# Optimization experiments

Hardware: AMD Instinct MI355X
Metric: run time of the kernel (lower is better)

## Reference

```python
import jax, jax.numpy as jnp
import numpy as np

K = 3            # kernel_size
S = 4            # up_factor
VMAX = 1.0
TAU = 0.5
CENTER_BIAS = 2.5
SMOOTH_RES = 0.15
C_IN = 21
HIDDEN = 48
B_, H0, W0 = 4, 81, 81
CTR = K // 2      # = 1, also GL recursion depth M


def _dir_step_diff(k):
    """Precompute (base_pos - base_neg) per direction/step: [8, M+1, k, k]."""
    c = k // 2
    dirs = np.array([[1, 0], [1, 1], [0, 1], [-1, 1], [-1, 0], [-1, -1], [0, -1], [1, -1]], np.float32)
    dirs = dirs / (np.linalg.norm(dirs, axis=1, keepdims=True) + 1e-8)
    yy, xx = np.meshgrid(np.arange(k), np.arange(k), indexing='ij')
    rel = np.stack([yy - c, xx - c], -1).astype(np.float32)
    diff = np.zeros((8, c + 1, k, k), np.float32)
    for d in range(8):
        v = dirs[d]
        proj = rel[..., 0] * v[1] + rel[..., 1] * v[0]
        step = np.clip(np.round(proj), -c, c).astype(np.int64)
        for m in range(c + 1):
            diff[d, m] = (step == m).astype(np.float32) - (step == -m).astype(np.float32)
    return diff

DIFF = jnp.asarray(_dir_step_diff(K))  # [8, M+1, K, K]


def conv3x3(x, w, b):
    y = jax.lax.conv_general_dilated(x, w, (1, 1), 'SAME',
                                     dimension_numbers=('NCHW', 'OIHW', 'NCHW'))
    return y + b[None, :, None, None]


def bilinear_up(x, s):
    """F.interpolate(scale_factor=s, mode='bilinear', align_corners=True)."""
    B, C, h, w = x.shape
    H, W = h * s, w * s
    ys = jnp.linspace(0.0, h - 1.0, H)
    xs = jnp.linspace(0.0, w - 1.0, W)
    y0 = jnp.clip(jnp.floor(ys).astype(jnp.int32), 0, h - 2)
    x0 = jnp.clip(jnp.floor(xs).astype(jnp.int32), 0, w - 2)
    wy = (ys - y0)[:, None]
    wx = (xs - x0)[None, :]
    x00 = x[:, :, y0][:, :, :, x0]
    x01 = x[:, :, y0][:, :, :, x0 + 1]
    x10 = x[:, :, y0 + 1][:, :, :, x0]
    x11 = x[:, :, y0 + 1][:, :, :, x0 + 1]
    return (x00 * (1 - wy) * (1 - wx) + x01 * (1 - wy) * wx
            + x10 * wy * (1 - wx) + x11 * wy * wx)


def setup_inputs() -> dict:
    key = jax.random.key(0)
    ks = jax.random.split(key, 6)
    wn = lambda k, shape: jax.random.normal(k, shape, jnp.float32) * 0.05
    return {
        'x': jax.random.normal(ks[0], (B_, C_IN, H0, W0), jnp.float32),
        'w1o': wn(ks[1], (HIDDEN, C_IN, 3, 3)), 'b1o': jnp.zeros((HIDDEN,), jnp.float32),
        'w2o': wn(ks[2], (8, HIDDEN, 3, 3)), 'b2o': jnp.zeros((8,), jnp.float32),
        'w1g': wn(ks[3], (HIDDEN, C_IN, 3, 3)), 'b1g': jnp.zeros((HIDDEN,), jnp.float32),
        'w2g': wn(ks[4], (1, HIDDEN, 3, 3)), 'b2g': jnp.zeros((1,), jnp.float32),
        'beta': jnp.asarray(1.6, jnp.float32),
    }


def reference(x, w1o, b1o, w2o, b2o, w1g, b1g, w2g, b2g, beta):
    B, C, h, w = x.shape
    c = CTR
    # heads
    raw_v = conv3x3(jax.nn.relu(conv3x3(x, w1o, b1o)), w2o, b2o)          # [B,8,h,w]
    g = jax.nn.sigmoid(conv3x3(jax.nn.relu(conv3x3(x, w1g, b1g)), w2g, b2g))  # [B,1,h,w]
    v = VMAX * jnp.tanh(raw_v)
    # Gruenwald-Letnikov coefficients, M = center (=1 for k=3)
    coeffs = [jnp.ones_like(v)]
    wm = coeffs[0]
    for m in range(1, c + 1):
        wm = wm * (v - m + 1.0) / m * -1.0
        coeffs.append(wm)
    coeff = jnp.stack(coeffs, axis=2)                                      # [B,8,M+1,h,w]
    # direction kernels, averaged over the 8 directions
    ker = jnp.einsum('bdmhw,dmkl->bklhw', coeff, DIFF) / 8.0               # [B,K,K,h,w]
    mask_pre = ker.reshape(B, K * K, h, w)
    ci = c * K + c
    # NOTE: torch adds center_bias in-place on a view of ker -> ker itself is biased too
    mask_pre = mask_pre.at[:, ci].add(CENTER_BIAS)
    ker_b = mask_pre.reshape(B, K, K, h, w)
    mask_lp = jax.nn.softmax(mask_pre / TAU, axis=1)                       # [B,9,h,w]
    # unfold 3x3 window with reflect padding
    xp = jnp.pad(x, ((0, 0), (0, 0), (c, c), (c, c)), mode='reflect')
    patches = jnp.stack([xp[:, :, i:i + h, j:j + w]
                         for i in range(K) for j in range(K)], axis=2)     # [B,C,9,h,w]
    rep2 = lambda a, ax: jnp.repeat(jnp.repeat(a, S, axis=ax), S, axis=ax + 1)
    neigh = rep2(patches, 3)                                               # [B,C,9,H,W]
    mask_lp_u = rep2(mask_lp, 2)                                           # [B,9,H,W]
    g_up = rep2(g, 2)                                                      # [B,1,H,W]
    x_up = bilinear_up(x, S)                                               # [B,C,H,W]
    y_lp_out = jnp.einsum('bcnHW,bnHW->bcHW', neigh, mask_lp_u)
    lam = SMOOTH_RES * (1.0 - g_up)
    y_lp = x_up + lam * (y_lp_out - x_up)
    # highpass branch (mode='both')
    ker_hp = ker_b - ker_b.mean(axis=(1, 2), keepdims=True)
    ker_hp = ker_hp / (jnp.abs(ker_hp).sum(axis=(1, 2), keepdims=True) + 1e-8)
    mask_hp = rep2(ker_hp.reshape(B, K * K, h, w), 2)
    y_hp = jnp.einsum('bcnHW,bnHW->bcHW', neigh, mask_hp)
    y = y_lp + jnp.tanh(beta) * g_up * y_hp
    return (y, v, g_up)
```

## Files before the change

### kernel.cpp

```cpp
#include <hip/hip_runtime.h>
#include <math.h>

#define B_N   4
#define CIN   21
#define HIDC  48
#define H0    81
#define NP    6561
#define HH    324
#define NPH   104976

__device__ __forceinline__ float tanh_fast(float x) {
    float e = __expf(2.f * x);
    return 1.f - 2.f / (e + 1.f);
}

__global__ __launch_bounds__(256) void k1_conv1(
    const float* __restrict__ x,
    const float* __restrict__ w1o, const float* __restrict__ b1o,
    const float* __restrict__ w1g, const float* __restrict__ b1g,
    float* __restrict__ hid_o, float* __restrict__ hid_g)
{
    __shared__ __align__(16) float wt[189 * 12];
    __shared__ float bs[12];
    const int tid = threadIdx.x;
    const int grp = blockIdx.y;
    const int b   = blockIdx.z;
    const bool head_o = (grp < 4);
    const int ocb = (grp & 3) * 12;
    const float* wsrc = head_o ? w1o : w1g;
    for (int i = tid; i < 189 * 12; i += 256) {
        const int ict = i / 12, oc = i - ict * 12;
        wt[i] = wsrc[(ocb + oc) * 189 + ict];
    }
    if (tid < 12) bs[tid] = (head_o ? b1o : b1g)[ocb + tid];
    __syncthreads();

    const int px = blockIdx.x * 256 + tid;
    const bool valid = (px < NP);
    const int oy = px / H0, ox = px - oy * H0;
    const float* xb = x + (size_t)b * CIN * NP;

    float acc[12];
    #pragma unroll
    for (int j = 0; j < 12; j++) acc[j] = bs[j];

    for (int ic = 0; ic < CIN; ic++) {
        const float* xc = xb + ic * NP;
        float xv[9];
        #pragma unroll
        for (int ky = 0; ky < 3; ky++) {
            const int iy = oy + ky - 1;
            const bool rok = valid && ((unsigned)iy < (unsigned)H0);
            #pragma unroll
            for (int kx = 0; kx < 3; kx++) {
                const int ix = ox + kx - 1;
                const bool ok = rok && ((unsigned)ix < (unsigned)H0);
                xv[ky * 3 + kx] = ok ? xc[iy * H0 + ix] : 0.f;
            }
        }
        #pragma unroll
        for (int tap = 0; tap < 9; tap++) {
            const float4 w0 = *(const float4*)&wt[(ic * 9 + tap) * 12];
            const float4 w1 = *(const float4*)&wt[(ic * 9 + tap) * 12 + 4];
            const float4 w2 = *(const float4*)&wt[(ic * 9 + tap) * 12 + 8];
            const float wj[12] = {w0.x, w0.y, w0.z, w0.w, w1.x, w1.y, w1.z, w1.w,
                                  w2.x, w2.y, w2.z, w2.w};
            const float xvt = xv[tap];
            #pragma unroll
            for (int j = 0; j < 12; j++) acc[j] = fmaf(xvt, wj[j], acc[j]);
        }
    }

    if (valid) {
        float* outp = (head_o ? hid_o : hid_g) + ((size_t)b * HIDC + ocb) * NP + px;
        #pragma unroll
        for (int j = 0; j < 12; j++) outp[j * NP] = fmaxf(acc[j], 0.f);
    }
}

__global__ __launch_bounds__(256) void k2_conv2_masks(
    const float* __restrict__ hid_o, const float* __restrict__ hid_g,
    const float* __restrict__ w2o, const float* __restrict__ b2o,
    const float* __restrict__ w2g, const float* __restrict__ b2g,
    float* __restrict__ v_out,
    float* __restrict__ g_buf, float* __restrict__ m_lp, float* __restrict__ m_hp)
{
    __shared__ __align__(16) float wo_s[HIDC * 9 * 8];
    __shared__ float wg_s[HIDC * 9];
    __shared__ float red[4][32][12];
    __shared__ float res_s[32][28];
    const int tid = threadIdx.x;
    const int b = blockIdx.y;

    for (int i = tid; i < HIDC * 9 * 8; i += 256) {
        const int d = i / (HIDC * 9), r = i - d * (HIDC * 9);
        wo_s[r * 8 + d] = w2o[i];
    }
    for (int i = tid; i < HIDC * 9; i += 256) wg_s[i] = w2g[i];
    __syncthreads();

    const int pxl = tid & 31;
    const int s   = tid >> 5;
    const int w   = tid >> 6;
    const int px  = blockIdx.x * 32 + pxl;
    const bool valid = (px < NP);
    const int oy = px / H0, ox = px - oy * H0;
    const int ic0 = s * 6;
    const float* po = hid_o + ((size_t)b * HIDC + ic0) * NP;
    const float* pg = hid_g + ((size_t)b * HIDC + ic0) * NP;

    float a[8] = {0.f, 0.f, 0.f, 0.f, 0.f, 0.f, 0.f, 0.f};
    float ag = 0.f;

    #pragma unroll 1
    for (int ky = 0; ky < 3; ky++) {
        const int iy = oy + ky - 1;
        const bool rok = valid && ((unsigned)iy < (unsigned)H0);
        #pragma unroll
        for (int kx = 0; kx < 3; kx++) {
            const int ix = ox + kx - 1;
            const bool ok = rok && ((unsigned)ix < (unsigned)H0);
            const int off = iy * H0 + ix;
            const int tap = ky * 3 + kx;
            #pragma unroll
            for (int j = 0; j < 6; j++) {
                const float vo = ok ? po[j * NP + off] : 0.f;
                const float vg = ok ? pg[j * NP + off] : 0.f;
                const int wb = ((ic0 + j) * 9 + tap) * 8;
                const float4 wA = *(const float4*)&wo_s[wb];
                const float4 wB = *(const float4*)&wo_s[wb + 4];
                a[0] = fmaf(vo, wA.x, a[0]); a[1] = fmaf(vo, wA.y, a[1]);
                a[2] = fmaf(vo, wA.z, a[2]); a[3] = fmaf(vo, wA.w, a[3]);
                a[4] = fmaf(vo, wB.x, a[4]); a[5] = fmaf(vo, wB.y, a[5]);
                a[6] = fmaf(vo, wB.z, a[6]); a[7] = fmaf(vo, wB.w, a[7]);
                ag = fmaf(vg, wg_s[(ic0 + j) * 9 + tap], ag);
            }
        }
    }

    #pragma unroll
    for (int n = 0; n < 8; n++) a[n] += __shfl_xor(a[n], 32);
    ag += __shfl_xor(ag, 32);
    if ((tid & 32) == 0) {
        #pragma unroll
        for (int n = 0; n < 8; n++) red[w][pxl][n] = a[n];
        red[w][pxl][8] = ag;
    }
    __syncthreads();

    if (tid < 32 && valid) {
        float v[8];
        #pragma unroll
        for (int n = 0; n < 8; n++)
            v[n] = tanh_fast(red[0][tid][n] + red[1][tid][n] + red[2][tid][n]
                             + red[3][tid][n] + b2o[n]);
        const float agf = red[0][tid][8] + red[1][tid][8] + red[2][tid][8]
                        + red[3][tid][8] + b2g[0];
        const float g = 1.f / (1.f + __expf(-agf));

        constexpr float DT[8][9] = {
            {-1, 0, 1, -1, 0, 1, -1, 0, 1},
            {-1,-1, 0, -1, 0, 1,  0, 1, 1},
            {-1,-1,-1,  0, 0, 0,  1, 1, 1},
            { 0,-1,-1,  1, 0,-1,  1, 1, 0},
            { 1, 0,-1,  1, 0,-1,  1, 0,-1},
            { 1, 1, 0,  1, 0,-1,  0,-1,-1},
            { 1, 1, 1,  0, 0, 0, -1,-1,-1},
            { 0, 1, 1, -1, 0, 1, -1,-1, 0}};
        float ker[9];
        #pragma unroll
        for (int n = 0; n < 9; n++) {
            float t = 0.f;
            #pragma unroll
            for (int d = 0; d < 8; d++) t += v[d] * DT[d][n];
            ker[n] = -0.125f * t;
        }
        ker[4] += 2.5f;
        float mx = ker[0];
        #pragma unroll
        for (int n = 1; n < 9; n++) mx = fmaxf(mx, ker[n]);
        float exn[9], sum = 0.f;
        #pragma unroll
        for (int n = 0; n < 9; n++) { exn[n] = __expf((ker[n] - mx) * 2.0f); sum += exn[n]; }
        const float rs = 1.f / sum;
        float mean = 0.f;
        #pragma unroll
        for (int n = 0; n < 9; n++) mean += ker[n];
        mean *= (1.f / 9.f);
        float den = 1e-8f;
        #pragma unroll
        for (int n = 0; n < 9; n++) den += fabsf(ker[n] - mean);
        const float rd = 1.f / den;

        #pragma unroll
        for (int n = 0; n < 8; n++) res_s[tid][n] = v[n];
        res_s[tid][8] = g;
        #pragma unroll
        for (int n = 0; n < 9; n++) {
            res_s[tid][9 + n]  = exn[n] * rs;
            res_s[tid][18 + n] = (ker[n] - mean) * rd;
        }
    }
    __syncthreads();

    const int px0 = blockIdx.x * 32;
    for (int j = tid; j < 27 * 32; j += 256) {
        const int plane = j >> 5, pl = j & 31;
        const int p = px0 + pl;
        if (p >= NP) continue;
        const float val = res_s[pl][plane];
        float* dst;
        if (plane < 8)        dst = v_out + ((size_t)b * 8 + plane) * NP;
        else if (plane == 8)  dst = g_buf + (size_t)b * NP;
        else if (plane < 18)  dst = m_lp + ((size_t)b * 9 + (plane - 9)) * NP;
        else                  dst = m_hp + ((size_t)b * 9 + (plane - 18)) * NP;
        dst[p] = val;
    }
}

__global__ __launch_bounds__(256) void k4_up(
    const float* __restrict__ x, const float* __restrict__ g_buf,
    const float* __restrict__ m_lp, const float* __restrict__ m_hp,
    const float* __restrict__ beta,
    float* __restrict__ y_out, float* __restrict__ gup_out)
{
    __shared__ float ml_s[9][81];
    __shared__ float mh_s[9][81];
    __shared__ float g_s[81];
    __shared__ float xrow[3][11][84];
    __shared__ float alp_s[11][84];
    __shared__ float ahp_s[11][84];
    const int tid  = threadIdx.x;
    const int h0r  = blockIdx.x;
    const int ygrp = blockIdx.y;
    const int b    = blockIdx.z;
    const int c0   = ygrp * 11;
    const int nc   = (ygrp == 0) ? 11 : 10;

    const int rb = h0r * H0;
    for (int i = tid; i < 19 * 81; i += 256) {
        const int pl = i / 81, wq = i - pl * 81;
        if (pl < 9)       ml_s[pl][wq] = m_lp[((size_t)b * 9 + pl) * NP + rb + wq];
        else if (pl < 18) mh_s[pl - 9][wq] = m_hp[((size_t)b * 9 + (pl - 9)) * NP + rb + wq];
        else              g_s[wq] = g_buf[(size_t)b * NP + rb + wq];
    }
    const int r0 = (h0r == 0) ? 1 : h0r - 1;
    const int r2 = (h0r == H0 - 1) ? H0 - 2 : h0r + 1;
    const int rr[3] = {r0, h0r, r2};
    for (int i = tid; i < 3 * nc * 81; i += 256) {
        const int t = i / (nc * 81), rem = i - t * nc * 81;
        const int cc = rem / 81, wq = rem - cc * 81;
        xrow[t][cc][wq] = x[((size_t)b * CIN + c0 + cc) * NP + rr[t] * H0 + wq];
    }
    __syncthreads();

    for (int i = tid; i < nc * 81; i += 256) {
        const int cc = i / 81, wq = i - cc * 81;
        const int xm = (wq == 0) ? 1 : wq - 1;
        const int xp = (wq == H0 - 1) ? H0 - 2 : wq + 1;
        float alp = 0.f, ahp = 0.f;
        #pragma unroll
        for (int t = 0; t < 3; t++) {
            const float p0 = xrow[t][cc][xm];
            const float p1 = xrow[t][cc][wq];
            const float p2 = xrow[t][cc][xp];
            alp += p0 * ml_s[t * 3 + 0][wq] + p1 * ml_s[t * 3 + 1][wq] + p2 * ml_s[t * 3 + 2][wq];
            ahp += p0 * mh_s[t * 3 + 0][wq] + p1 * mh_s[t * 3 + 1][wq] + p2 * mh_s[t * 3 + 2][wq];
        }
        alp_s[cc][wq] = alp;
        ahp_s[cc][wq] = ahp;
    }
    __syncthreads();

    const float tb = tanh_fast(beta[0]);
    for (int i = tid; i < 11 * 4 * 81; i += 256) {
        const int pl = i / 324, rem = i - pl * 324;
        const int dh = rem / 81, wq = rem - dh * 81;
        const int H = h0r * 4 + dh;
        if (ygrp == 1 && pl == 10) {
            const float g = g_s[wq];
            *reinterpret_cast<float4*>(gup_out + (size_t)b * NPH + H * HH + wq * 4) =
                make_float4(g, g, g, g);
            continue;
        }
        const int cc = pl;
        const int c = c0 + pl;
        const float g = g_s[wq];
        const float lam = 0.15f * (1.f - g);
        const float gh = tb * g;
        const float alp = alp_s[cc][wq];
        const float ahp = ahp_s[cc][wq];
        const float ysf = (float)H * (80.f / 323.f);
        int y0 = (int)ysf;
        if (y0 > H0 - 2) y0 = H0 - 2;
        const float wy = ysf - (float)y0;
        const int sy = y0 - h0r + 1;
        const int xm = (wq == 0) ? 1 : wq - 1;
        const int xp = (wq == H0 - 1) ? H0 - 2 : wq + 1;
        const float a0 = xrow[sy][cc][(wq == 0) ? 0 : xm];
        const float a1 = xrow[sy][cc][wq];
        const float a2 = xrow[sy][cc][(wq == H0 - 1) ? H0 - 1 : xp];
        const float b0 = xrow[sy + 1][cc][(wq == 0) ? 0 : xm];
        const float b1 = xrow[sy + 1][cc][wq];
        const float b2 = xrow[sy + 1][cc][(wq == H0 - 1) ? H0 - 1 : xp];
        float res[4];
        #pragma unroll
        for (int k = 0; k < 4; k++) {
            const int W = wq * 4 + k;
            const float xsf = (float)W * (80.f / 323.f);
            int x0 = (int)xsf;
            if (x0 > H0 - 2) x0 = H0 - 2;
            const float wx = xsf - (float)x0;
            const int sx = x0 - wq + 1;
            const float top = (sx == 0) ? a0 + (a1 - a0) * wx : a1 + (a2 - a1) * wx;
            const float bot = (sx == 0) ? b0 + (b1 - b0) * wx : b1 + (b2 - b1) * wx;
            const float xup = top + (bot - top) * wy;
            res[k] = xup + lam * (alp - xup) + gh * ahp;
        }
        *reinterpret_cast<float4*>(y_out + ((size_t)b * CIN + c) * NPH + H * HH + wq * 4) =
            make_float4(res[0], res[1], res[2], res[3]);
    }
}

extern "C" void kernel_launch(void* const* d_in, const int* in_sizes, int n_in,
                              void* d_out, int out_size, void* d_ws, size_t ws_size,
                              hipStream_t stream)
{
    const float* x    = (const float*)d_in[0];
    const float* w1o  = (const float*)d_in[1];
    const float* b1o  = (const float*)d_in[2];
    const float* w2o  = (const float*)d_in[3];
    const float* b2o  = (const float*)d_in[4];
    const float* w1g  = (const float*)d_in[5];
    const float* b1g  = (const float*)d_in[6];
    const float* w2g  = (const float*)d_in[7];
    const float* b2g  = (const float*)d_in[8];
    const float* beta = (const float*)d_in[9];
    float* out = (float*)d_out;
    float* wsf = (float*)d_ws;

    float* hid_o = wsf;
    float* hid_g = hid_o + (size_t)B_N * HIDC * NP;
    float* m_lp  = hid_g + (size_t)B_N * HIDC * NP;
    float* m_hp  = m_lp + (size_t)B_N * 9 * NP;
    float* g_buf = m_hp + (size_t)B_N * 9 * NP;

    float* y_out = out;
    float* v_out = out + (size_t)B_N * CIN * NPH;
    float* gup   = v_out + (size_t)B_N * 8 * NP;

    k1_conv1<<<dim3((NP + 255) / 256, 8, B_N), 256, 0, stream>>>(
        x, w1o, b1o, w1g, b1g, hid_o, hid_g);
    k2_conv2_masks<<<dim3((NP + 31) / 32, B_N), 256, 0, stream>>>(
        hid_o, hid_g, w2o, b2o, w2g, b2g, v_out, g_buf, m_lp, m_hp);
    k4_up<<<dim3(H0, 2, B_N), 256, 0, stream>>>(x, g_buf, m_lp, m_hp, beta, y_out, gup);
}
```

Measured before the change: 152.8 us.

## Fuse conv2/mask kernel with upsampling kernel per low-res row half

Merges the second conv plus mask computation into the upsampling kernel. Each block now covers one low-res row half (41 pixels) for all 21 channels, so the lp/hp masks and gate stay in shared memory and never go through global workspace. This removes one launch and the global round trip for the masks. In exchange only 246 of 256 threads do conv2 work, and the grid of 648 blocks each reload the conv2 weights and all channel rows, so parallelism and occupancy shift.

```diff
diff --git a/kernel.cpp b/kernel.cpp
--- a/kernel.cpp
+++ b/kernel.cpp
@@ -78,85 +78,103 @@
     }
 }
 
-__global__ __launch_bounds__(256) void k2_conv2_masks(
+__global__ __launch_bounds__(256) void k24_conv2_up(
+    const float* __restrict__ x,
     const float* __restrict__ hid_o, const float* __restrict__ hid_g,
     const float* __restrict__ w2o, const float* __restrict__ b2o,
     const float* __restrict__ w2g, const float* __restrict__ b2g,
-    float* __restrict__ v_out,
-    float* __restrict__ g_buf, float* __restrict__ m_lp, float* __restrict__ m_hp)
+    const float* __restrict__ beta,
+    float* __restrict__ v_out, float* __restrict__ y_out,
+    float* __restrict__ gup_out)
 {
     __shared__ __align__(16) float wo_s[HIDC * 9 * 8];
     __shared__ float wg_s[HIDC * 9];
-    __shared__ float red[4][32][12];
-    __shared__ float res_s[32][28];
-    const int tid = threadIdx.x;
-    const int b = blockIdx.y;
+    __shared__ float xrow[3][CIN][84];
+    __shared__ float red_u[6 * 41 * 9];
+    __shared__ float ml_s[9][41];
+    __shared__ float mh_s[9][41];
+    __shared__ float g_s[41];
+
+    const int tid  = threadIdx.x;
+    const int h0r  = blockIdx.x;
+    const int half = blockIdx.y;
+    const int b    = blockIdx.z;
+    const int wq0  = half * 41;
 
     for (int i = tid; i < HIDC * 9 * 8; i += 256) {
         const int d = i / (HIDC * 9), r = i - d * (HIDC * 9);
         wo_s[r * 8 + d] = w2o[i];
     }
     for (int i = tid; i < HIDC * 9; i += 256) wg_s[i] = w2g[i];
-    __syncthreads();
-
-    const int pxl = tid & 31;
-    const int s   = tid >> 5;
-    const int w   = tid >> 6;
-    const int px  = blockIdx.x * 32 + pxl;
-    const bool valid = (px < NP);
-    const int oy = px / H0, ox = px - oy * H0;
-    const int ic0 = s * 6;
-    const float* po = hid_o + ((size_t)b * HIDC + ic0) * NP;
-    const float* pg = hid_g + ((size_t)b * HIDC + ic0) * NP;
-
-    float a[8] = {0.f, 0.f, 0.f, 0.f, 0.f, 0.f, 0.f, 0.f};
-    float ag = 0.f;
-
-    #pragma unroll 1
-    for (int ky = 0; ky < 3; ky++) {
-        const int iy = oy + ky - 1;
-        const bool rok = valid && ((unsigned)iy < (unsigned)H0);
-        #pragma unroll
-        for (int kx = 0; kx < 3; kx++) {
-            const int ix = ox + kx - 1;
-            const bool ok = rok && ((unsigned)ix < (unsigned)H0);
-            const int off = iy * H0 + ix;
-            const int tap = ky * 3 + kx;
-            #pragma unroll
-            for (int j = 0; j < 6; j++) {
-                const float vo = ok ? po[j * NP + off] : 0.f;
-                const float vg = ok ? pg[j * NP + off] : 0.f;
-                const int wb = ((ic0 + j) * 9 + tap) * 8;
-                const float4 wA = *(const float4*)&wo_s[wb];
-                const float4 wB = *(const float4*)&wo_s[wb + 4];
-                a[0] = fmaf(vo, wA.x, a[0]); a[1] = fmaf(vo, wA.y, a[1]);
-                a[2] = fmaf(vo, wA.z, a[2]); a[3] = fmaf(vo, wA.w, a[3]);
-                a[4] = fmaf(vo, wB.x, a[4]); a[5] = fmaf(vo, wB.y, a[5]);
-                a[6] = fmaf(vo, wB.z, a[6]); a[7] = fmaf(vo, wB.w, a[7]);
-                ag = fmaf(vg, wg_s[(ic0 + j) * 9 + tap], ag);
+
+    const int r0 = (h0r == 0) ? 1 : h0r - 1;
+    const int r2 = (h0r == H0 - 1) ? H0 - 2 : h0r + 1;
+    const int rr[3] = {r0, h0r, r2};
+    for (int i = tid; i < 3 * CIN * H0; i += 256) {
+        const int t3 = i / (CIN * H0), rem = i - t3 * CIN * H0;
+        const int cc = rem / H0, wq = rem - cc * H0;
+        xrow[t3][cc][wq] = x[((size_t)b * CIN + cc) * NP + rr[t3] * H0 + wq];
+    }
+    __syncthreads();
+
+    {
+        const int grp = tid / 41;
+        const int pxl = tid - grp * 41;
+        const int wq  = wq0 + pxl;
+        const bool cactive = (grp < 6) && (wq < H0);
+        if (cactive) {
+            const int ic0 = grp * 8;
+            const float* po = hid_o + ((size_t)b * HIDC + ic0) * NP;
+            const float* pg = hid_g + ((size_t)b * HIDC + ic0) * NP;
+            float a[8] = {0.f, 0.f, 0.f, 0.f, 0.f, 0.f, 0.f, 0.f};
+            float ag = 0.f;
+            #pragma unroll
+            for (int ky = 0; ky < 3; ky++) {
+                const int iy = h0r + ky - 1;
+                const bool rok = ((unsigned)iy < (unsigned)H0);
+                #pragma unroll
+                for (int kx = 0; kx < 3; kx++) {
+                    const int ix = wq + kx - 1;
+                    const bool ok = rok && ((unsigned)ix < (unsigned)H0);
+                    const int off = iy * H0 + ix;
+                    const int tap = ky * 3 + kx;
+                    #pragma unroll
+                    for (int j = 0; j < 8; j++) {
+                        const float vo = ok ? po[j * NP + off] : 0.f;
+                        const float vg = ok ? pg[j * NP + off] : 0.f;
+                        const int wb = ((ic0 + j) * 9 + tap) * 8;
+                        const float4 wA = *(const float4*)&wo_s[wb];
+                        const float4 wB = *(const float4*)&wo_s[wb + 4];
+                        a[0] = fmaf(vo, wA.x, a[0]); a[1] = fmaf(vo, wA.y, a[1]);
+                        a[2] = fmaf(vo, wA.z, a[2]); a[3] = fmaf(vo, wA.w, a[3]);
+                        a[4] = fmaf(vo, wB.x, a[4]); a[5] = fmaf(vo, wB.y, a[5]);
+                        a[6] = fmaf(vo, wB.z, a[6]); a[7] = fmaf(vo, wB.w, a[7]);
+                        ag = fmaf(vg, wg_s[(ic0 + j) * 9 + tap], ag);
+                    }
+                }
             }
-        }
-    }
-
-    #pragma unroll
-    for (int n = 0; n < 8; n++) a[n] += __shfl_xor(a[n], 32);
-    ag += __shfl_xor(ag, 32);
-    if ((tid & 32) == 0) {
-        #pragma unroll
-        for (int n = 0; n < 8; n++) red[w][pxl][n] = a[n];
-        red[w][pxl][8] = ag;
-    }
-    __syncthreads();
-
-    if (tid < 32 && valid) {
+            float* rp = &red_u[(grp * 41 + pxl) * 9];
+            #pragma unroll
+            for (int n = 0; n < 8; n++) rp[n] = a[n];
+            rp[8] = ag;
+        }
+    }
+    __syncthreads();
+
+    if (tid < 41 && (wq0 + tid) < H0) {
+        const int wq = wq0 + tid;
+        float s[9];
+        #pragma unroll
+        for (int n = 0; n < 9; n++) {
+            float t = 0.f;
+            #pragma unroll
+            for (int g = 0; g < 6; g++) t += red_u[(g * 41 + tid) * 9 + n];
+            s[n] = t;
+        }
         float v[8];
         #pragma unroll
-        for (int n = 0; n < 8; n++)
-            v[n] = tanh_fast(red[0][tid][n] + red[1][tid][n] + red[2][tid][n]
-                             + red[3][tid][n] + b2o[n]);
-        const float agf = red[0][tid][8] + red[1][tid][8] + red[2][tid][8]
-                        + red[3][tid][8] + b2g[0];
-        const float g = 1.f / (1.f + __expf(-agf));
+        for (int n = 0; n < 8; n++) v[n] = tanh_fast(s[n] + b2o[n]);
+        const float g = 1.f / (1.f + __expf(-(s[8] + b2g[0])));
 
         constexpr float DT[8][9] = {
             {-1, 0, 1, -1, 0, 1, -1, 0, 1},
@@ -193,103 +211,58 @@
         const float rd = 1.f / den;
 
         #pragma unroll
-        for (int n = 0; n < 8; n++) res_s[tid][n] = v[n];
-        res_s[tid][8] = g;
-        #pragma unroll
         for (int n = 0; n < 9; n++) {
-            res_s[tid][9 + n]  = exn[n] * rs;
-            res_s[tid][18 + n] = (ker[n] - mean) * rd;
-        }
-    }
-    __syncthreads();
-
-    const int px0 = blockIdx.x * 32;
-    for (int j = tid; j < 27 * 32; j += 256) {
-        const int plane = j >> 5, pl = j & 31;
-        const int p = px0 + pl;
-        if (p >= NP) continue;
-        const float val = res_s[pl][plane];
-        float* dst;
-        if (plane < 8)        dst = v_out + ((size_t)b * 8 + plane) * NP;
-        else if (plane == 8)  dst = g_buf + (size_t)b * NP;
-        else if (plane < 18)  dst = m_lp + ((size_t)b * 9 + (plane - 9)) * NP;
-        else                  dst = m_hp + ((size_t)b * 9 + (plane - 18)) * NP;
-        dst[p] = val;
-    }
-}
-
-__global__ __launch_bounds__(256) void k4_up(
-    const float* __restrict__ x, const float* __restrict__ g_buf,
-    const float* __restrict__ m_lp, const float* __restrict__ m_hp,
-    const float* __restrict__ beta,
-    float* __restrict__ y_out, float* __restrict__ gup_out)
-{
-    __shared__ float ml_s[9][81];
-    __shared__ float mh_s[9][81];
-    __shared__ float g_s[81];
-    __shared__ float xrow[3][11][84];
-    __shared__ float alp_s[11][84];
-    __shared__ float ahp_s[11][84];
-    const int tid  = threadIdx.x;
-    const int h0r  = blockIdx.x;
-    const int ygrp = blockIdx.y;
-    const int b    = blockIdx.z;
-    const int c0   = ygrp * 11;
-    const int nc   = (ygrp == 0) ? 11 : 10;
-
-    const int rb = h0r * H0;
-    for (int i = tid; i < 19 * 81; i += 256) {
-        const int pl = i / 81, wq = i - pl * 81;
-        if (pl < 9)       ml_s[pl][wq] = m_lp[((size_t)b * 9 + pl) * NP + rb + wq];
-        else if (pl < 18) mh_s[pl - 9][wq] = m_hp[((size_t)b * 9 + (pl - 9)) * NP + rb + wq];
-        else              g_s[wq] = g_buf[(size_t)b * NP + rb + wq];
-    }
-    const int r0 = (h0r == 0) ? 1 : h0r - 1;
-    const int r2 = (h0r == H0 - 1) ? H0 - 2 : h0r + 1;
-    const int rr[3] = {r0, h0r, r2};
-    for (int i = tid; i < 3 * nc * 81; i += 256) {
-        const int t = i / (nc * 81), rem = i - t * nc * 81;
-        const int cc = rem / 81, wq = rem - cc * 81;
-        xrow[t][cc][wq] = x[((size_t)b * CIN + c0 + cc) * NP + rr[t] * H0 + wq];
-    }
-    __syncthreads();
-
-    for (int i = tid; i < nc * 81; i += 256) {
-        const int cc = i / 81, wq = i - cc * 81;
+            ml_s[n][tid] = exn[n] * rs;
+            mh_s[n][tid] = (ker[n] - mean) * rd;
+        }
+        g_s[tid] = g;
+        #pragma unroll
+        for (int n = 0; n < 8; n++)
+            v_out[((size_t)b * 8 + n) * NP + h0r * H0 + wq] = v[n];
+    }
+    __syncthreads();
+
+    float* alp_s = red_u;
+    float* ahp_s = red_u + CIN * 41;
+    for (int i = tid; i < CIN * 41; i += 256) {
+        const int cc = i / 41, pxl = i - cc * 41;
+        const int wq = wq0 + pxl;
+        if (wq >= H0) continue;
         const int xm = (wq == 0) ? 1 : wq - 1;
         const int xp = (wq == H0 - 1) ? H0 - 2 : wq + 1;
         float alp = 0.f, ahp = 0.f;
         #pragma unroll
-        for (int t = 0; t < 3; t++) {
-            const float p0 = xrow[t][cc][xm];
-            const float p1 = xrow[t][cc][wq];
-            const float p2 = xrow[t][cc][xp];
-            alp += p0 * ml_s[t * 3 + 0][wq] + p1 * ml_s[t * 3 + 1][wq] + p2 * ml_s[t * 3 + 2][wq];
-            ahp += p0 * mh_s[t * 3 + 0][wq] + p1 * mh_s[t * 3 + 1][wq] + p2 * mh_s[t * 3 + 2][wq];
-        }
-        alp_s[cc][wq] = alp;
-        ahp_s[cc][wq] = ahp;
+        for (int t3 = 0; t3 < 3; t3++) {
+            const float p0 = xrow[t3][cc][xm];
+            const float p1 = xrow[t3][cc][wq];
+            const float p2 = xrow[t3][cc][xp];
+            alp += p0 * ml_s[t3 * 3 + 0][pxl] + p1 * ml_s[t3 * 3 + 1][pxl] + p2 * ml_s[t3 * 3 + 2][pxl];
+            ahp += p0 * mh_s[t3 * 3 + 0][pxl] + p1 * mh_s[t3 * 3 + 1][pxl] + p2 * mh_s[t3 * 3 + 2][pxl];
+        }
+        alp_s[cc * 41 + pxl] = alp;
+        ahp_s[cc * 41 + pxl] = ahp;
     }
     __syncthreads();
 
     const float tb = tanh_fast(beta[0]);
-    for (int i = tid; i < 11 * 4 * 81; i += 256) {
-        const int pl = i / 324, rem = i - pl * 324;
-        const int dh = rem / 81, wq = rem - dh * 81;
+    for (int i = tid; i < 22 * 4 * 41; i += 256) {
+        const int pl = i / 164, rem = i - pl * 164;
+        const int dh = rem / 41, pxl = rem - dh * 41;
+        const int wq = wq0 + pxl;
+        if (wq >= H0) continue;
         const int H = h0r * 4 + dh;
-        if (ygrp == 1 && pl == 10) {
-            const float g = g_s[wq];
+        if (pl == 21) {
+            const float g = g_s[pxl];
             *reinterpret_cast<float4*>(gup_out + (size_t)b * NPH + H * HH + wq * 4) =
                 make_float4(g, g, g, g);
             continue;
         }
         const int cc = pl;
-        const int c = c0 + pl;
-        const float g = g_s[wq];
+        const float g = g_s[pxl];
         const float lam = 0.15f * (1.f - g);
         const float gh = tb * g;
-        const float alp = alp_s[cc][wq];
-        const float ahp = ahp_s[cc][wq];
+        const float alp = alp_s[cc * 41 + pxl];
+        const float ahp = ahp_s[cc * 41 + pxl];
         const float ysf = (float)H * (80.f / 323.f);
         int y0 = (int)ysf;
         if (y0 > H0 - 2) y0 = H0 - 2;
@@ -317,7 +290,7 @@
             const float xup = top + (bot - top) * wy;
             res[k] = xup + lam * (alp - xup) + gh * ahp;
         }
-        *reinterpret_cast<float4*>(y_out + ((size_t)b * CIN + c) * NPH + H * HH + wq * 4) =
+        *reinterpret_cast<float4*>(y_out + ((size_t)b * CIN + cc) * NPH + H * HH + wq * 4) =
             make_float4(res[0], res[1], res[2], res[3]);
     }
 }
@@ -341,9 +314,6 @@
 
     float* hid_o = wsf;
     float* hid_g = hid_o + (size_t)B_N * HIDC * NP;
-    float* m_lp  = hid_g + (size_t)B_N * HIDC * NP;
-    float* m_hp  = m_lp + (size_t)B_N * 9 * NP;
-    float* g_buf = m_hp + (size_t)B_N * 9 * NP;
 
     float* y_out = out;
     float* v_out = out + (size_t)B_N * CIN * NPH;
@@ -351,7 +321,6 @@
 
     k1_conv1<<<dim3((NP + 255) / 256, 8, B_N), 256, 0, stream>>>(
         x, w1o, b1o, w1g, b1g, hid_o, hid_g);
-    k2_conv2_masks<<<dim3((NP + 31) / 32, B_N), 256, 0, stream>>>(
-        hid_o, hid_g, w2o, b2o, w2g, b2g, v_out, g_buf, m_lp, m_hp);
-    k4_up<<<dim3(H0, 2, B_N), 256, 0, stream>>>(x, g_buf, m_lp, m_hp, beta, y_out, gup);
+    k24_conv2_up<<<dim3(H0, 2, B_N), 256, 0, stream>>>(
+        x, hid_o, hid_g, w2o, b2o, w2g, b2g, beta, v_out, y_out, gup);
 }
```

New measurement: 276.4 us. +80.8%, slower.

## Fuse conv2/mask kernel with upsampling kernel, dropping intermediate mask buffers

Applied to the files above, without the earlier changes.

Merges the second-conv/mask-generation kernel and the upsample/filter kernel into one kernel that works on 32-pixel tiles. Masks and gate stay in shared memory, and x neighbours are read straight from global memory. This removes a launch and the global write and read of the m_lp, m_hp and g buffers. In exchange, output writes become less contiguous (32 scattered pixels per block rather than full rows), and x is re-read from global without a shared row cache.

```diff
diff --git a/kernel.cpp b/kernel.cpp
--- a/kernel.cpp
+++ b/kernel.cpp
@@ -78,17 +78,21 @@
     }
 }
 
-__global__ __launch_bounds__(256) void k2_conv2_masks(
+__global__ __launch_bounds__(256) void k2up(
+    const float* __restrict__ x,
     const float* __restrict__ hid_o, const float* __restrict__ hid_g,
     const float* __restrict__ w2o, const float* __restrict__ b2o,
     const float* __restrict__ w2g, const float* __restrict__ b2g,
-    float* __restrict__ v_out,
-    float* __restrict__ g_buf, float* __restrict__ m_lp, float* __restrict__ m_hp)
+    const float* __restrict__ beta,
+    float* __restrict__ v_out, float* __restrict__ y_out,
+    float* __restrict__ gup_out)
 {
     __shared__ __align__(16) float wo_s[HIDC * 9 * 8];
     __shared__ float wg_s[HIDC * 9];
     __shared__ float red[4][32][12];
-    __shared__ float res_s[32][28];
+    __shared__ float res_s[32][29];
+    __shared__ float alp2[CIN][32];
+    __shared__ float ahp2[CIN][32];
     const int tid = threadIdx.x;
     const int b = blockIdx.y;
 
@@ -102,7 +106,8 @@
     const int pxl = tid & 31;
     const int s   = tid >> 5;
     const int w   = tid >> 6;
-    const int px  = blockIdx.x * 32 + pxl;
+    const int px0 = blockIdx.x * 32;
+    const int px  = px0 + pxl;
     const bool valid = (px < NP);
     const int oy = px / H0, ox = px - oy * H0;
     const int ic0 = s * 6;
@@ -203,121 +208,88 @@
     }
     __syncthreads();
 
-    const int px0 = blockIdx.x * 32;
-    for (int j = tid; j < 27 * 32; j += 256) {
-        const int plane = j >> 5, pl = j & 31;
+    {
+        const int plane = tid >> 5, pl = tid & 31;
+        const int p = px0 + pl;
+        if (p < NP) v_out[((size_t)b * 8 + plane) * NP + p] = res_s[pl][plane];
+    }
+
+    for (int i = tid; i < CIN * 32; i += 256) {
+        const int c = i >> 5, pl = i & 31;
         const int p = px0 + pl;
         if (p >= NP) continue;
-        const float val = res_s[pl][plane];
-        float* dst;
-        if (plane < 8)        dst = v_out + ((size_t)b * 8 + plane) * NP;
-        else if (plane == 8)  dst = g_buf + (size_t)b * NP;
-        else if (plane < 18)  dst = m_lp + ((size_t)b * 9 + (plane - 9)) * NP;
-        else                  dst = m_hp + ((size_t)b * 9 + (plane - 18)) * NP;
-        dst[p] = val;
-    }
-}
-
-__global__ __launch_bounds__(256) void k4_up(
-    const float* __restrict__ x, const float* __restrict__ g_buf,
-    const float* __restrict__ m_lp, const float* __restrict__ m_hp,
-    const float* __restrict__ beta,
-    float* __restrict__ y_out, float* __restrict__ gup_out)
-{
-    __shared__ float ml_s[9][81];
-    __shared__ float mh_s[9][81];
-    __shared__ float g_s[81];
-    __shared__ float xrow[3][11][84];
-    __shared__ float alp_s[11][84];
-    __shared__ float ahp_s[11][84];
-    const int tid  = threadIdx.x;
-    const int h0r  = blockIdx.x;
-    const int ygrp = blockIdx.y;
-    const int b    = blockIdx.z;
-    const int c0   = ygrp * 11;
-    const int nc   = (ygrp == 0) ? 11 : 10;
-
-    const int rb = h0r * H0;
-    for (int i = tid; i < 19 * 81; i += 256) {
-        const int pl = i / 81, wq = i - pl * 81;
-        if (pl < 9)       ml_s[pl][wq] = m_lp[((size_t)b * 9 + pl) * NP + rb + wq];
-        else if (pl < 18) mh_s[pl - 9][wq] = m_hp[((size_t)b * 9 + (pl - 9)) * NP + rb + wq];
-        else              g_s[wq] = g_buf[(size_t)b * NP + rb + wq];
-    }
-    const int r0 = (h0r == 0) ? 1 : h0r - 1;
-    const int r2 = (h0r == H0 - 1) ? H0 - 2 : h0r + 1;
-    const int rr[3] = {r0, h0r, r2};
-    for (int i = tid; i < 3 * nc * 81; i += 256) {
-        const int t = i / (nc * 81), rem = i - t * nc * 81;
-        const int cc = rem / 81, wq = rem - cc * 81;
-        xrow[t][cc][wq] = x[((size_t)b * CIN + c0 + cc) * NP + rr[t] * H0 + wq];
-    }
-    __syncthreads();
-
-    for (int i = tid; i < nc * 81; i += 256) {
-        const int cc = i / 81, wq = i - cc * 81;
-        const int xm = (wq == 0) ? 1 : wq - 1;
-        const int xp = (wq == H0 - 1) ? H0 - 2 : wq + 1;
+        const int py = p / H0, pxc = p - py * H0;
+        const int ym = (py == 0) ? 1 : py - 1;
+        const int yp = (py == H0 - 1) ? H0 - 2 : py + 1;
+        const int xm = (pxc == 0) ? 1 : pxc - 1;
+        const int xp = (pxc == H0 - 1) ? H0 - 2 : pxc + 1;
+        const float* xc = x + ((size_t)b * CIN + c) * NP;
+        const int ry[3] = {ym, py, yp};
+        const int rx[3] = {xm, pxc, xp};
         float alp = 0.f, ahp = 0.f;
         #pragma unroll
         for (int t = 0; t < 3; t++) {
-            const float p0 = xrow[t][cc][xm];
-            const float p1 = xrow[t][cc][wq];
-            const float p2 = xrow[t][cc][xp];
-            alp += p0 * ml_s[t * 3 + 0][wq] + p1 * ml_s[t * 3 + 1][wq] + p2 * ml_s[t * 3 + 2][wq];
-            ahp += p0 * mh_s[t * 3 + 0][wq] + p1 * mh_s[t * 3 + 1][wq] + p2 * mh_s[t * 3 + 2][wq];
-        }
-        alp_s[cc][wq] = alp;
-        ahp_s[cc][wq] = ahp;
+            const float* xr = xc + ry[t] * H0;
+            #pragma unroll
+            for (int u = 0; u < 3; u++) {
+                const float xv = xr[rx[u]];
+                alp = fmaf(xv, res_s[pl][9 + t * 3 + u], alp);
+                ahp = fmaf(xv, res_s[pl][18 + t * 3 + u], ahp);
+            }
+        }
+        alp2[c][pl] = alp;
+        ahp2[c][pl] = ahp;
     }
     __syncthreads();
 
     const float tb = tanh_fast(beta[0]);
-    for (int i = tid; i < 11 * 4 * 81; i += 256) {
-        const int pl = i / 324, rem = i - pl * 324;
-        const int dh = rem / 81, wq = rem - dh * 81;
-        const int H = h0r * 4 + dh;
-        if (ygrp == 1 && pl == 10) {
-            const float g = g_s[wq];
-            *reinterpret_cast<float4*>(gup_out + (size_t)b * NPH + H * HH + wq * 4) =
+    for (int i = tid; i < 22 * 4 * 32; i += 256) {
+        const int pl  = i >> 7;
+        const int rem = i & 127;
+        const int dh  = rem >> 5, pp = rem & 31;
+        const int p = px0 + pp;
+        if (p >= NP) continue;
+        const int py = p / H0, pxc = p - py * H0;
+        const int H = py * 4 + dh;
+        const float g = res_s[pp][8];
+        if (pl == 21) {
+            *reinterpret_cast<float4*>(gup_out + (size_t)b * NPH + H * HH + pxc * 4) =
                 make_float4(g, g, g, g);
             continue;
         }
-        const int cc = pl;
-        const int c = c0 + pl;
-        const float g = g_s[wq];
+        const int c = pl;
         const float lam = 0.15f * (1.f - g);
         const float gh = tb * g;
-        const float alp = alp_s[cc][wq];
-        const float ahp = ahp_s[cc][wq];
+        const float alp = alp2[c][pp];
+        const float ahp = ahp2[c][pp];
         const float ysf = (float)H * (80.f / 323.f);
         int y0 = (int)ysf;
         if (y0 > H0 - 2) y0 = H0 - 2;
         const float wy = ysf - (float)y0;
-        const int sy = y0 - h0r + 1;
-        const int xm = (wq == 0) ? 1 : wq - 1;
-        const int xp = (wq == H0 - 1) ? H0 - 2 : wq + 1;
-        const float a0 = xrow[sy][cc][(wq == 0) ? 0 : xm];
-        const float a1 = xrow[sy][cc][wq];
-        const float a2 = xrow[sy][cc][(wq == H0 - 1) ? H0 - 1 : xp];
-        const float b0 = xrow[sy + 1][cc][(wq == 0) ? 0 : xm];
-        const float b1 = xrow[sy + 1][cc][wq];
-        const float b2 = xrow[sy + 1][cc][(wq == H0 - 1) ? H0 - 1 : xp];
+        const float* xc = x + ((size_t)b * CIN + c) * NP;
+        const int cm = (pxc == 0) ? 0 : pxc - 1;
+        const int cp = (pxc == H0 - 1) ? H0 - 1 : pxc + 1;
+        const float a0 = xc[y0 * H0 + cm];
+        const float a1 = xc[y0 * H0 + pxc];
+        const float a2 = xc[y0 * H0 + cp];
+        const float b0 = xc[(y0 + 1) * H0 + cm];
+        const float b1 = xc[(y0 + 1) * H0 + pxc];
+        const float b2 = xc[(y0 + 1) * H0 + cp];
         float res[4];
         #pragma unroll
         for (int k = 0; k < 4; k++) {
-            const int W = wq * 4 + k;
+            const int W = pxc * 4 + k;
             const float xsf = (float)W * (80.f / 323.f);
             int x0 = (int)xsf;
             if (x0 > H0 - 2) x0 = H0 - 2;
             const float wx = xsf - (float)x0;
-            const int sx = x0 - wq + 1;
-            const float top = (sx == 0) ? a0 + (a1 - a0) * wx : a1 + (a2 - a1) * wx;
-            const float bot = (sx == 0) ? b0 + (b1 - b0) * wx : b1 + (b2 - b1) * wx;
-            const float xup = top + (bot - top) * wy;
-            res[k] = xup + lam * (alp - xup) + gh * ahp;
-        }
-        *reinterpret_cast<float4*>(y_out + ((size_t)b * CIN + c) * NPH + H * HH + wq * 4) =
+            const int sx = x0 - pxc + 1;
+            const float top = (sx == 0) ? fmaf(a1 - a0, wx, a0) : fmaf(a2 - a1, wx, a1);
+            const float bot = (sx == 0) ? fmaf(b1 - b0, wx, b0) : fmaf(b2 - b1, wx, b1);
+            const float xup = fmaf(bot - top, wy, top);
+            res[k] = fmaf(lam, alp - xup, xup) + gh * ahp;
+        }
+        *reinterpret_cast<float4*>(y_out + ((size_t)b * CIN + c) * NPH + H * HH + pxc * 4) =
             make_float4(res[0], res[1], res[2], res[3]);
     }
 }
@@ -341,9 +313,6 @@
 
     float* hid_o = wsf;
     float* hid_g = hid_o + (size_t)B_N * HIDC * NP;
-    float* m_lp  = hid_g + (size_t)B_N * HIDC * NP;
-    float* m_hp  = m_lp + (size_t)B_N * 9 * NP;
-    float* g_buf = m_hp + (size_t)B_N * 9 * NP;
 
     float* y_out = out;
     float* v_out = out + (size_t)B_N * CIN * NPH;
@@ -351,7 +320,6 @@
 
     k1_conv1<<<dim3((NP + 255) / 256, 8, B_N), 256, 0, stream>>>(
         x, w1o, b1o, w1g, b1g, hid_o, hid_g);
-    k2_conv2_masks<<<dim3((NP + 31) / 32, B_N), 256, 0, stream>>>(
-        hid_o, hid_g, w2o, b2o, w2g, b2g, v_out, g_buf, m_lp, m_hp);
-    k4_up<<<dim3(H0, 2, B_N), 256, 0, stream>>>(x, g_buf, m_lp, m_hp, beta, y_out, gup);
+    k2up<<<dim3((NP + 31) / 32, B_N), 256, 0, stream>>>(
+        x, hid_o, hid_g, w2o, b2o, w2g, b2g, beta, v_out, y_out, gup);
 }
```

New measurement: 146.1 us. 1.05x faster.
